# Optimization experiments

Hardware: AMD Instinct MI355X
Metric: run time of the kernel (lower is better)

Reference implementation:

```python
import jax, jax.numpy as jnp
import numpy as np

N_NODES = 100000
N_EDGES = 600000
D = 128
NUM_RELS = 200


def setup_inputs() -> dict:
    key = jax.random.key(0)
    ks = jax.random.split(key, 12)
    s = 1.0 / np.sqrt(D)
    return {
        "h": jax.random.normal(ks[0], (N_NODES, D), jnp.float32),
        "prev_h": jax.random.normal(ks[1], (N_NODES, D), jnp.float32),
        "emb_rel": jax.random.normal(ks[2], (NUM_RELS, D), jnp.float32),
        "norm": jax.random.uniform(ks[3], (N_NODES, 1), jnp.float32),
        "weight_neighbor": jax.random.normal(ks[4], (D, D), jnp.float32) * s,
        "loop_weight": jax.random.normal(ks[5], (D, D), jnp.float32) * s,
        "evolve_loop_weight": jax.random.normal(ks[6], (D, D), jnp.float32) * s,
        "skip_connect_weight": jax.random.normal(ks[7], (D, D), jnp.float32) * s,
        "skip_connect_bias": jnp.zeros((D,), jnp.float32),
        "src": jax.random.randint(ks[8], (N_EDGES,), 0, N_NODES, jnp.int64),
        "dst": jax.random.randint(ks[9], (N_EDGES,), 0, N_NODES, jnp.int64),
        "etype": jax.random.randint(ks[10], (N_EDGES,), 0, NUM_RELS, jnp.int64),
    }


def reference(h, prev_h, emb_rel, norm, weight_neighbor, loop_weight,
              evolve_loop_weight, skip_connect_weight, skip_connect_bias,
              src, dst, etype):
    n = h.shape[0]
    # self-loop message: nodes with in-degree > 0 use loop_weight, else evolve_loop_weight
    in_deg = jax.ops.segment_sum(jnp.ones_like(dst, dtype=jnp.float32), dst,
                                 num_segments=n)  # [N]
    loop_message = jnp.where(in_deg[:, None] > 0,
                             h @ loop_weight,
                             h @ evolve_loop_weight)  # [N, D]
    # skip gate from previous layer hidden state
    skip_weight = jax.nn.sigmoid(prev_h @ skip_connect_weight + skip_connect_bias)
    # msg_func: gather src node feats + relation embedding, per-edge GEMM
    msg = (h[src] + emb_rel[etype]) @ weight_neighbor  # [E, D]
    # fn.sum scatter aggregation, then apply_func: multiply by node norm
    agg = jax.ops.segment_sum(msg, dst, num_segments=n)  # [N, D]
    node_repr = agg * norm
    # skip_connect (prev_h non-empty) + self_loop branch
    node_repr = node_repr + loop_message
    node_repr = skip_weight * node_repr + (1.0 - skip_weight) * prev_h
    # activation
    return jax.nn.relu(node_repr)
```

## Files before the change

### kernel.cpp

```cpp
#include <hip/hip_runtime.h>

#define DD 128

typedef __attribute__((ext_vector_type(8))) short short8;
typedef __attribute__((ext_vector_type(4))) float f32x4;
typedef __attribute__((ext_vector_type(4))) int i32x4;

__device__ __forceinline__ unsigned short f2bf(float f) {
    union { float f; unsigned int i; } c; c.f = f;
    unsigned int x = c.i;
    return (unsigned short)((x + 0x7fffu + ((x >> 16) & 1u)) >> 16);
}
__device__ __forceinline__ float bfu(unsigned short u) {
    union { unsigned int i; float f; } c; c.i = ((unsigned int)u) << 16; return c.f;
}
__device__ __forceinline__ void gload_lds16(const void* g, void* l) {
    __builtin_amdgcn_global_load_lds(
        (const __attribute__((address_space(1))) unsigned int*)g,
        (__attribute__((address_space(3))) unsigned int*)l, 16, 0, 0);
}
__device__ __forceinline__ int idx_at(const int* p, int e, int is64) {
    return is64 ? p[2 * e] : p[e];
}
__device__ __forceinline__ int block_is64(const int* dst, int nE, int* s_flag) {
    if (threadIdx.x == 0) *s_flag = 0;
    __syncthreads();
    int w = 2 * (int)threadIdx.x + 1;
    if (threadIdx.x < 128 && w < nE && dst[w] != 0) atomicOr(s_flag, 1);
    __syncthreads();
    return !*s_flag;
}

__global__ __launch_bounds__(256) void prep_k(
    const float* __restrict__ h,
    const float* __restrict__ W0, const float* __restrict__ W1,
    const float* __restrict__ W2, const float* __restrict__ emb,
    const int* __restrict__ dst,
    unsigned short* __restrict__ hB,
    unsigned short* __restrict__ embB, unsigned short* __restrict__ Wt,
    int* __restrict__ deg, int nN, int nEmbEl, int nE) {
    int tid = threadIdx.x;
    int bid = blockIdx.x;
    int nHistB = (nE + 1023) / 1024;
    if (bid < nHistB) {
        __shared__ int s_flag;
        int is64 = block_is64(dst, nE, &s_flag);
        int e0 = bid * 1024 + tid * 4;
        #pragma unroll
        for (int j = 0; j < 4; ++j) {
            int e = e0 + j;
            if (e < nE) atomicAdd(deg + idx_at(dst, e, is64), 1);
        }
        return;
    }
    bid -= nHistB;
    int totalH = nN * DD;
    int nConvH = (totalH + 8191) / 8192;
    if (bid < nConvH) {
        int base0 = bid * 8192;
        if (base0 + 8192 <= totalH) {
            int base = base0 + tid * 8;
            f32x4 x[4][2];
            #pragma unroll
            for (int i = 0; i < 4; ++i) {
                x[i][0] = *(const f32x4*)(h + base + i * 2048);
                x[i][1] = *(const f32x4*)(h + base + i * 2048 + 4);
            }
            #pragma unroll
            for (int i = 0; i < 4; ++i) {
                short8 p;
                #pragma unroll
                for (int j = 0; j < 4; ++j) {
                    p[j]     = (short)f2bf(x[i][0][j]);
                    p[4 + j] = (short)f2bf(x[i][1][j]);
                }
                *(short8*)(hB + base + i * 2048) = p;
            }
        } else {
            #pragma unroll
            for (int i = 0; i < 4; ++i) {
                int b2 = base0 + i * 2048 + tid * 8;
                if (b2 + 8 <= totalH) {
                    f32x4 x0 = *(const f32x4*)(h + b2);
                    f32x4 x1 = *(const f32x4*)(h + b2 + 4);
                    short8 p;
                    #pragma unroll
                    for (int j = 0; j < 4; ++j) {
                        p[j]     = (short)f2bf(x0[j]);
                        p[4 + j] = (short)f2bf(x1[j]);
                    }
                    *(short8*)(hB + b2) = p;
                } else {
                    for (int j = b2; j < totalH && j < b2 + 8; ++j)
                        hB[j] = f2bf(h[j]);
                }
            }
        }
        return;
    }
    bid -= nConvH;
    if (bid < 48) {
        const float* Ws[3] = {W0, W1, W2};
        int w = bid >> 4, chunk = bid & 15;
        unsigned short* T = Wt + w * (DD * DD);
        #pragma unroll
        for (int i = 0; i < 4; ++i) {
            int t = chunk * 1024 + i * 256 + tid;
            int n = t >> 7, k = t & 127;
            T[t] = f2bf(Ws[w][k * DD + n]);
        }
        return;
    }
    bid -= 48;
    int base = bid * 2048 + tid * 8;
    if (base + 8 <= nEmbEl) {
        f32x4 x0 = *(const f32x4*)(emb + base);
        f32x4 x1 = *(const f32x4*)(emb + base + 4);
        short8 p;
        #pragma unroll
        for (int j = 0; j < 4; ++j) {
            p[j]     = (short)f2bf(x0[j]);
            p[4 + j] = (short)f2bf(x1[j]);
        }
        *(short8*)(embB + base) = p;
    } else {
        for (int j = base; j < nEmbEl; ++j) embB[j] = f2bf(emb[j]);
    }
}

__global__ __launch_bounds__(1024) void scan1_k(const int* deg, int* off, int* bsum,
                                                int nN) {
    __shared__ int s[1024];
    int t = threadIdx.x, i = blockIdx.x * 1024 + t;
    int v = (i < nN) ? deg[i] : 0;
    s[t] = v;
    __syncthreads();
    for (int d = 1; d < 1024; d <<= 1) {
        int x = (t >= d) ? s[t - d] : 0;
        __syncthreads();
        s[t] += x;
        __syncthreads();
    }
    if (i < nN) off[i] = s[t] - v;
    if (t == 1023) bsum[blockIdx.x] = s[1023];
}

__global__ __launch_bounds__(1024) void scan23_k(const int* bsum, int* off,
                                                 int* cursor, int nN, int nB) {
    __shared__ int s[1024];
    int t = threadIdx.x;
    s[t] = (t < nB) ? bsum[t] : 0;
    __syncthreads();
    for (int d = 1; d < 1024; d <<= 1) {
        int x = (t >= d) ? s[t - d] : 0;
        __syncthreads();
        s[t] += x;
        __syncthreads();
    }
    int base = (blockIdx.x == 0) ? 0 : s[blockIdx.x - 1];
    int i = blockIdx.x * 1024 + t;
    if (i < nN) {
        int o = off[i] + base;
        off[i] = o;
        cursor[i] = o;
    }
}

__global__ __launch_bounds__(256) void sort_k(const int* src, const int* dst,
                                              const int* et, int nE,
                                              int* cursor, unsigned int* edges) {
    __shared__ int s_flag;
    int is64 = block_is64(dst, nE, &s_flag);
    int e = blockIdx.x * 256 + threadIdx.x;
    if (e >= nE) return;
    int d = idx_at(dst, e, is64);
    int pos = atomicAdd(cursor + d, 1);
    edges[pos] = (unsigned int)idx_at(src, e, is64) |
                 ((unsigned int)idx_at(et, e, is64) << 17);
}

__global__ __launch_bounds__(256) void gather_k(
    const unsigned short* __restrict__ hB, const unsigned short* __restrict__ embB,
    const unsigned int* __restrict__ edges, const int* __restrict__ off,
    const int* __restrict__ deg, const float* __restrict__ normv,
    char* __restrict__ aggP, int nN) {
    int lane = threadIdx.x & 63;
    int v = blockIdx.x * 4 + (threadIdx.x >> 6);
    if (v >= nN) return;
    int slot = lane >> 4, l16 = lane & 15;
    int b = off[v], n = deg[v];
    float a[8] = {0.f, 0.f, 0.f, 0.f, 0.f, 0.f, 0.f, 0.f};
    for (int base = 0; base < n; base += 8) {
        int m0 = base + slot, m1 = base + 4 + slot;
        bool v0 = m0 < n, v1 = m1 < n;
        unsigned int w0 = 0, w1 = 0;
        if (v0) w0 = edges[b + m0];
        if (v1) w1 = edges[b + m1];
        short8 hv0, rv0, hv1, rv1;
        if (v0) {
            hv0 = *(const short8*)(hB + (size_t)(w0 & 0x1FFFFu) * DD + l16 * 8);
            rv0 = *(const short8*)(embB + (size_t)(w0 >> 17) * DD + l16 * 8);
        }
        if (v1) {
            hv1 = *(const short8*)(hB + (size_t)(w1 & 0x1FFFFu) * DD + l16 * 8);
            rv1 = *(const short8*)(embB + (size_t)(w1 >> 17) * DD + l16 * 8);
        }
        if (v0) {
            #pragma unroll
            for (int j = 0; j < 8; ++j)
                a[j] += bfu((unsigned short)hv0[j]) + bfu((unsigned short)rv0[j]);
        }
        if (v1) {
            #pragma unroll
            for (int j = 0; j < 8; ++j)
                a[j] += bfu((unsigned short)hv1[j]) + bfu((unsigned short)rv1[j]);
        }
    }
    #pragma unroll
    for (int j = 0; j < 8; ++j) {
        a[j] += __shfl_xor(a[j], 16);
        a[j] += __shfl_xor(a[j], 32);
    }
    if (slot == 0) {
        float nm = normv[v];
        short8 p;
        #pragma unroll
        for (int j = 0; j < 8; ++j) p[j] = (short)f2bf(a[j] * nm);
        *(short8*)(aggP + (size_t)v * 512 + l16 * 16) = p;
    }
}

__global__ __launch_bounds__(256, 1) void fused_k(
    const unsigned short* __restrict__ hB,
    const float* __restrict__ prevh,
    const float* __restrict__ bias,
    const char* __restrict__ aggP,
    const unsigned short* __restrict__ Wt,
    float* __restrict__ out, int nN, int nTiles) {
    extern __shared__ unsigned short lds[];
    const int lane = threadIdx.x & 63;
    const int wv = threadIdx.x >> 6;
    const int q = lane >> 4, cl = lane & 15;
    const int ncb = wv * 32;
    const int stride = gridDim.x;

    int t = blockIdx.x;
    if (t >= nTiles) return;

    short8 bn[4][2], bl[4][2], bs[4][2];
    #pragma unroll
    for (int ks = 0; ks < 4; ++ks)
        #pragma unroll
        for (int nt = 0; nt < 2; ++nt) {
            int n = (ncb + nt * 16 + cl) * DD + ks * 32 + q * 8;
            bn[ks][nt] = *(const short8*)(Wt + n);
            bl[ks][nt] = *(const short8*)(Wt + DD * DD + n);
            bs[ks][nt] = *(const short8*)(Wt + 2 * DD * DD + n);
        }
    const float b0 = bias[ncb + cl], b1 = bias[ncb + 16 + cl];

    const int r0 = lane >> 4;
    const int c16 = lane & 15;

    {
        int node_base = t * 64;
        #pragma unroll
        for (int it = 0; it < 4; ++it) {
            int r = it * 16 + wv * 4 + r0;
            int row = node_base + r; if (row > nN - 1) row = nN - 1;
            int sw = (c16 ^ (r & 15)) << 4;
            char* bptr = (char*)lds + (it * 16 + wv * 4) * 256;
            gload_lds16(aggP + (size_t)row * 512 + sw, bptr);
            gload_lds16((const char*)hB + (size_t)row * 256 + sw, bptr + 16384);
        }
        f32x4 p0[4], p1[4];
        #pragma unroll
        for (int it = 0; it < 4; ++it) {
            int pos = it * 512 + lane * 8;
            int node = node_base + wv * 16 + (pos >> 7);
            if (node > nN - 1) node = nN - 1;
            const float* g = prevh + (size_t)node * DD + (pos & 127);
            p0[it] = *(const f32x4*)g;
            p1[it] = *(const f32x4*)(g + 4);
        }
        #pragma unroll
        for (int it = 0; it < 4; ++it) {
            int pos = it * 512 + lane * 8;
            int r = wv * 16 + (pos >> 7);
            int c = (pos & 127) >> 3;
            short8 p;
            #pragma unroll
            for (int j = 0; j < 4; ++j) {
                p[j]     = (short)f2bf(p0[it][j]);
                p[4 + j] = (short)f2bf(p1[it][j]);
            }
            *(short8*)((char*)lds + 32768 + r * 256 + ((c ^ (r & 15)) << 4)) = p;
        }
    }
    __syncthreads();

    int cur = 0;
    for (;;) {
        int node_base = t * 64;
        int tn = t + stride;
        bool more = (tn < nTiles);

        f32x4 p0[4], p1[4];
        if (more) {
            int nb2 = tn * 64;
            char* dbuf = (char*)lds + (cur ^ 1) * 49152;
            #pragma unroll
            for (int it = 0; it < 4; ++it) {
                int r = it * 16 + wv * 4 + r0;
                int row = nb2 + r; if (row > nN - 1) row = nN - 1;
                int sw = (c16 ^ (r & 15)) << 4;
                char* bptr = dbuf + (it * 16 + wv * 4) * 256;
                gload_lds16(aggP + (size_t)row * 512 + sw, bptr);
                gload_lds16((const char*)hB + (size_t)row * 256 + sw, bptr + 16384);
            }
            #pragma unroll
            for (int it = 0; it < 4; ++it) {
                int pos = it * 512 + lane * 8;
                int node = nb2 + wv * 16 + (pos >> 7);
                if (node > nN - 1) node = nN - 1;
                const float* g = prevh + (size_t)node * DD + (pos & 127);
                p0[it] = *(const f32x4*)g;
                p1[it] = *(const f32x4*)(g + 4);
            }
        }

        const unsigned short* lA = lds + cur * 24576;
        const unsigned short* lH = lA + 8192;
        const unsigned short* lP = lA + 16384;

        f32x4 accM[4][2], accG[4][2];
        #pragma unroll
        for (int mt = 0; mt < 4; ++mt)
            #pragma unroll
            for (int nt = 0; nt < 2; ++nt) {
                accM[mt][nt] = (f32x4){0.f, 0.f, 0.f, 0.f};
                accG[mt][nt] = (f32x4){0.f, 0.f, 0.f, 0.f};
            }
        #pragma unroll
        for (int ks = 0; ks < 4; ++ks) {
            int swz = ((ks * 4 + q) ^ cl) << 3;
            #pragma unroll
            for (int mt = 0; mt < 4; ++mt) {
                int off = (mt * 16 + cl) * 128 + swz;
                short8 aA = *(const short8*)(lA + off);
                short8 aH = *(const short8*)(lH + off);
                short8 aP = *(const short8*)(lP + off);
                #pragma unroll
                for (int nt = 0; nt < 2; ++nt) {
                    accM[mt][nt] = __builtin_amdgcn_mfma_f32_16x16x32_bf16(
                        aA, bn[ks][nt], accM[mt][nt], 0, 0, 0);
                    accM[mt][nt] = __builtin_amdgcn_mfma_f32_16x16x32_bf16(
                        aH, bl[ks][nt], accM[mt][nt], 0, 0, 0);
                    accG[mt][nt] = __builtin_amdgcn_mfma_f32_16x16x32_bf16(
                        aP, bs[ks][nt], accG[mt][nt], 0, 0, 0);
                }
            }
        }

        #pragma unroll
        for (int mt = 0; mt < 4; ++mt) {
            #pragma unroll
            for (int r = 0; r < 4; ++r) {
                int nrow = mt * 16 + q * 4 + r;
                int node = node_base + nrow;
                if (node >= nN) continue;
                #pragma unroll
                for (int nt = 0; nt < 2; ++nt) {
                    int col = ncb + nt * 16 + cl;
                    float pv = bfu(lP[nrow * 128 +
                                      ((((col >> 3) ^ (nrow & 15)) << 3) | (col & 7))]);
                    float sg = 1.0f / (1.0f + __expf(-(accG[mt][nt][r] +
                                                       (nt ? b1 : b0))));
                    float o  = sg * accM[mt][nt][r] + (1.0f - sg) * pv;
                    out[(size_t)node * DD + col] = (o > 0.f ? o : 0.f);
                }
            }
        }

        if (more) {
            char* dbuf = (char*)lds + (cur ^ 1) * 49152;
            #pragma unroll
            for (int it = 0; it < 4; ++it) {
                int pos = it * 512 + lane * 8;
                int r = wv * 16 + (pos >> 7);
                int c = (pos & 127) >> 3;
                short8 p;
                #pragma unroll
                for (int j = 0; j < 4; ++j) {
                    p[j]     = (short)f2bf(p0[it][j]);
                    p[4 + j] = (short)f2bf(p1[it][j]);
                }
                *(short8*)(dbuf + 32768 + r * 256 + ((c ^ (r & 15)) << 4)) = p;
            }
        }
        __syncthreads();
        if (!more) break;
        cur ^= 1;
        t = tn;
    }
}

__global__ __launch_bounds__(256) void fix_k(
    const float* __restrict__ h, const float* __restrict__ prevh,
    const float* __restrict__ bias, const float* __restrict__ We,
    const float* __restrict__ Wsk, const int* __restrict__ deg,
    float* __restrict__ out, int nN, int chunk) {
    __shared__ int list[256];
    __shared__ int cnt;
    __shared__ float hrow[DD], prow[DD], res[2][DD];
    int tid = threadIdx.x;
    int base = blockIdx.x * chunk;
    for (int c = base; c < base + chunk && c < nN; c += 256) {
        if (tid == 0) cnt = 0;
        __syncthreads();
        int v = c + tid;
        if (v < nN && v < base + chunk && deg[v] == 0)
            list[atomicAdd(&cnt, 1)] = v;
        __syncthreads();
        int m = cnt;
        for (int i = 0; i < m; ++i) {
            int node = list[i];
            if (tid < DD) hrow[tid] = h[(size_t)node * DD + tid];
            else prow[tid - DD] = prevh[(size_t)node * DD + tid - DD];
            __syncthreads();
            int col = tid & (DD - 1);
            int half = tid >> 7;
            const float* W = half ? Wsk : We;
            const float* x = half ? prow : hrow;
            float s = 0.f;
            for (int k = 0; k < DD; ++k) s += x[k] * W[k * DD + col];
            res[half][col] = s;
            __syncthreads();
            if (tid < DD) {
                float sg = 1.0f / (1.0f + __expf(-(res[1][col] + bias[col])));
                float o  = sg * res[0][col] + (1.0f - sg) * prow[col];
                out[(size_t)node * DD + col] = (o > 0.f ? o : 0.f);
            }
            __syncthreads();
        }
        __syncthreads();
    }
}

extern "C" void kernel_launch(void* const* d_in, const int* in_sizes, int n_in,
                              void* d_out, int out_size, void* d_ws, size_t ws_size,
                              hipStream_t stream) {
    const float* h     = (const float*)d_in[0];
    const float* prevh = (const float*)d_in[1];
    const float* emb   = (const float*)d_in[2];
    const float* normv = (const float*)d_in[3];
    const float* Wn    = (const float*)d_in[4];
    const float* Wl    = (const float*)d_in[5];
    const float* We    = (const float*)d_in[6];
    const float* Wsk   = (const float*)d_in[7];
    const float* bias  = (const float*)d_in[8];
    const int* src   = (const int*)d_in[9];
    const int* dst   = (const int*)d_in[10];
    const int* etype = (const int*)d_in[11];

    int nN = in_sizes[3];
    int nE = in_sizes[9];
    int nEmbEl = in_sizes[2];

    char* w = (char*)d_ws;
    size_t o = 0;
    unsigned short* Wt = (unsigned short*)(w + o);  o += 3 * DD * DD * 2;
    unsigned short* embB = (unsigned short*)(w + o); o += ((size_t)nEmbEl * 2 + 255) & ~(size_t)255;
    int* deg    = (int*)(w + o);  o += ((size_t)nN * 4 + 15) & ~(size_t)15;
    int* offA   = (int*)(w + o);  o += ((size_t)nN * 4 + 15) & ~(size_t)15;
    int* cursor = (int*)(w + o);  o += ((size_t)nN * 4 + 15) & ~(size_t)15;
    int* bsum   = (int*)(w + o);  o += 4096;
    unsigned int* edges = (unsigned int*)(w + o); o += ((size_t)nE * 4 + 15) & ~(size_t)15;
    unsigned short* hB = (unsigned short*)(w + o);

    int totalH = nN * DD;
    int nConvH = (totalH + 8191) / 8192;
    int nEmbB  = (nEmbEl + 2047) / 2048;
    int nHistB = (nE + 1023) / 1024;
    int nB = (nN + 1023) / 1024;
    int nTiles = (nN + 63) / 64;
    int fgrid2 = nTiles < 256 ? nTiles : 256;

    hipMemsetAsync(deg, 0, (size_t)nN * sizeof(int), stream);
    prep_k<<<nHistB + nConvH + 48 + nEmbB, 256, 0, stream>>>(
        h, Wn, Wl, Wsk, emb, dst, hB, embB, Wt, deg, nN, nEmbEl, nE);
    scan1_k<<<nB, 1024, 0, stream>>>(deg, offA, bsum, nN);
    scan23_k<<<nB, 1024, 0, stream>>>(bsum, offA, cursor, nN, nB);
    sort_k<<<(nE + 255) / 256, 256, 0, stream>>>(src, dst, etype, nE, cursor, edges);
    gather_k<<<(nN + 3) / 4, 256, 0, stream>>>(hB, embB, edges, offA, deg, normv,
                                               (char*)d_out, nN);
    fused_k<<<fgrid2, 256, 98304, stream>>>(hB, prevh, bias, (const char*)d_out,
                                            Wt, (float*)d_out, nN, nTiles);
    int fgrid = 256;
    int chunk = ((nN + fgrid * 256 - 1) / (fgrid * 256)) * 256;
    fix_k<<<fgrid, 256, 0, stream>>>(h, prevh, bias, We, Wsk, deg, (float*)d_out,
                                     nN, chunk);
    (void)ws_size; (void)n_in; (void)out_size;
}
```

Baseline: 311.8 us.

## Replace global-atomic edge sort with two-pass bucketed counting sort; shrink fused tiles

The per-edge scatter with a global atomic per destination node is replaced by a two-pass sort. The first pass does a block-local histogram over 128-node buckets, makes one global atomic per bucket and writes to a staging array. The second pass scatters within each bucket using LDS atomics. This cuts global atomic contention and makes the edge writes more local, at the cost of an extra pass over the edges and an extra staging buffer. Separately, the fused GEMM kernel moves to 32-row tiles with half the LDS and a 512-block grid, so two blocks can be resident per CU.

```diff
diff --git a/kernel.cpp b/kernel.cpp
--- a/kernel.cpp
+++ b/kernel.cpp
@@ -1,6 +1,7 @@
 #include <hip/hip_runtime.h>
 
 #define DD 128
+#define SCHUNK 4096
 
 typedef __attribute__((ext_vector_type(8))) short short8;
 typedef __attribute__((ext_vector_type(4))) float f32x4;
@@ -146,7 +147,7 @@
 }
 
 __global__ __launch_bounds__(1024) void scan23_k(const int* bsum, int* off,
-                                                 int* cursor, int nN, int nB) {
+                                                 int* cursorB, int nN, int nB) {
     __shared__ int s[1024];
     int t = threadIdx.x;
     s[t] = (t < nB) ? bsum[t] : 0;
@@ -162,21 +163,67 @@
     if (i < nN) {
         int o = off[i] + base;
         off[i] = o;
-        cursor[i] = o;
-    }
-}
-
-__global__ __launch_bounds__(256) void sort_k(const int* src, const int* dst,
-                                              const int* et, int nE,
-                                              int* cursor, unsigned int* edges) {
+        if ((i & 127) == 0) cursorB[i >> 7] = o;
+    }
+}
+
+__global__ __launch_bounds__(256) void sort1_k(
+    const int* __restrict__ src, const int* __restrict__ dst,
+    const int* __restrict__ et, int nE, int nBuck,
+    int* __restrict__ cursorB, unsigned int* __restrict__ staging) {
+    __shared__ int hist[2048];
+    __shared__ int rbase[2048];
+    __shared__ unsigned short ranks[SCHUNK];
     __shared__ int s_flag;
+    int tid = threadIdx.x;
     int is64 = block_is64(dst, nE, &s_flag);
-    int e = blockIdx.x * 256 + threadIdx.x;
-    if (e >= nE) return;
-    int d = idx_at(dst, e, is64);
-    int pos = atomicAdd(cursor + d, 1);
-    edges[pos] = (unsigned int)idx_at(src, e, is64) |
-                 ((unsigned int)idx_at(et, e, is64) << 17);
+    for (int i = tid; i < nBuck; i += 256) hist[i] = 0;
+    __syncthreads();
+    int cbase = blockIdx.x * SCHUNK;
+    #pragma unroll
+    for (int j = 0; j < SCHUNK / 256; ++j) {
+        int e = cbase + j * 256 + tid;
+        if (e < nE) {
+            int d = idx_at(dst, e, is64);
+            ranks[j * 256 + tid] = (unsigned short)atomicAdd(&hist[d >> 7], 1);
+        }
+    }
+    __syncthreads();
+    for (int b = tid; b < nBuck; b += 256) {
+        int c = hist[b];
+        if (c) rbase[b] = atomicAdd(cursorB + b, c);
+    }
+    __syncthreads();
+    #pragma unroll
+    for (int j = 0; j < SCHUNK / 256; ++j) {
+        int e = cbase + j * 256 + tid;
+        if (e < nE) {
+            int d = idx_at(dst, e, is64);
+            unsigned int wd = (unsigned int)idx_at(src, e, is64) |
+                              ((unsigned int)idx_at(et, e, is64) << 17) |
+                              ((unsigned int)(d & 127) << 25);
+            staging[rbase[d >> 7] + (int)ranks[j * 256 + tid]] = wd;
+        }
+    }
+}
+
+__global__ __launch_bounds__(256) void sort2_k(
+    const unsigned int* __restrict__ staging, const int* __restrict__ off,
+    int nN, int nE, unsigned int* __restrict__ edges) {
+    __shared__ int cur[128];
+    int b = blockIdx.x;
+    int first = b << 7;
+    int tid = threadIdx.x;
+    if (tid < 128 && first + tid < nN) cur[tid] = off[first + tid];
+    int rStart = off[first];
+    int nxt = first + 128;
+    int rEnd = (nxt < nN) ? off[nxt] : nE;
+    __syncthreads();
+    for (int i = rStart + tid; i < rEnd; i += 256) {
+        unsigned int wd = staging[i];
+        int p = atomicAdd(&cur[wd >> 25], 1);
+        edges[p] = wd & 0x1FFFFFFu;
+    }
 }
 
 __global__ __launch_bounds__(256) void gather_k(
@@ -230,7 +277,7 @@
     }
 }
 
-__global__ __launch_bounds__(256, 1) void fused_k(
+__global__ __launch_bounds__(256, 2) void fused_k(
     const unsigned short* __restrict__ hB,
     const float* __restrict__ prevh,
     const float* __restrict__ bias,
@@ -263,30 +310,30 @@
     const int c16 = lane & 15;
 
     {
-        int node_base = t * 64;
-        #pragma unroll
-        for (int it = 0; it < 4; ++it) {
+        int node_base = t * 32;
+        #pragma unroll
+        for (int it = 0; it < 2; ++it) {
             int r = it * 16 + wv * 4 + r0;
             int row = node_base + r; if (row > nN - 1) row = nN - 1;
             int sw = (c16 ^ (r & 15)) << 4;
             char* bptr = (char*)lds + (it * 16 + wv * 4) * 256;
             gload_lds16(aggP + (size_t)row * 512 + sw, bptr);
-            gload_lds16((const char*)hB + (size_t)row * 256 + sw, bptr + 16384);
-        }
-        f32x4 p0[4], p1[4];
-        #pragma unroll
-        for (int it = 0; it < 4; ++it) {
+            gload_lds16((const char*)hB + (size_t)row * 256 + sw, bptr + 8192);
+        }
+        f32x4 p0[2], p1[2];
+        #pragma unroll
+        for (int it = 0; it < 2; ++it) {
             int pos = it * 512 + lane * 8;
-            int node = node_base + wv * 16 + (pos >> 7);
+            int node = node_base + wv * 8 + (pos >> 7);
             if (node > nN - 1) node = nN - 1;
             const float* g = prevh + (size_t)node * DD + (pos & 127);
             p0[it] = *(const f32x4*)g;
             p1[it] = *(const f32x4*)(g + 4);
         }
         #pragma unroll
-        for (int it = 0; it < 4; ++it) {
+        for (int it = 0; it < 2; ++it) {
             int pos = it * 512 + lane * 8;
-            int r = wv * 16 + (pos >> 7);
+            int r = wv * 8 + (pos >> 7);
             int c = (pos & 127) >> 3;
             short8 p;
             #pragma unroll
@@ -294,34 +341,34 @@
                 p[j]     = (short)f2bf(p0[it][j]);
                 p[4 + j] = (short)f2bf(p1[it][j]);
             }
-            *(short8*)((char*)lds + 32768 + r * 256 + ((c ^ (r & 15)) << 4)) = p;
+            *(short8*)((char*)lds + 16384 + r * 256 + ((c ^ (r & 15)) << 4)) = p;
         }
     }
     __syncthreads();
 
     int cur = 0;
     for (;;) {
-        int node_base = t * 64;
+        int node_base = t * 32;
         int tn = t + stride;
         bool more = (tn < nTiles);
 
-        f32x4 p0[4], p1[4];
+        f32x4 p0[2], p1[2];
         if (more) {
-            int nb2 = tn * 64;
-            char* dbuf = (char*)lds + (cur ^ 1) * 49152;
-            #pragma unroll
-            for (int it = 0; it < 4; ++it) {
+            int nb2 = tn * 32;
+            char* dbuf = (char*)lds + (cur ^ 1) * 24576;
+            #pragma unroll
+            for (int it = 0; it < 2; ++it) {
                 int r = it * 16 + wv * 4 + r0;
                 int row = nb2 + r; if (row > nN - 1) row = nN - 1;
                 int sw = (c16 ^ (r & 15)) << 4;
                 char* bptr = dbuf + (it * 16 + wv * 4) * 256;
                 gload_lds16(aggP + (size_t)row * 512 + sw, bptr);
-                gload_lds16((const char*)hB + (size_t)row * 256 + sw, bptr + 16384);
-            }
-            #pragma unroll
-            for (int it = 0; it < 4; ++it) {
+                gload_lds16((const char*)hB + (size_t)row * 256 + sw, bptr + 8192);
+            }
+            #pragma unroll
+            for (int it = 0; it < 2; ++it) {
                 int pos = it * 512 + lane * 8;
-                int node = nb2 + wv * 16 + (pos >> 7);
+                int node = nb2 + wv * 8 + (pos >> 7);
                 if (node > nN - 1) node = nN - 1;
                 const float* g = prevh + (size_t)node * DD + (pos & 127);
                 p0[it] = *(const f32x4*)g;
@@ -329,13 +376,13 @@
             }
         }
 
-        const unsigned short* lA = lds + cur * 24576;
-        const unsigned short* lH = lA + 8192;
-        const unsigned short* lP = lA + 16384;
-
-        f32x4 accM[4][2], accG[4][2];
-        #pragma unroll
-        for (int mt = 0; mt < 4; ++mt)
+        const unsigned short* lA = lds + cur * 12288;
+        const unsigned short* lH = lA + 4096;
+        const unsigned short* lP = lA + 8192;
+
+        f32x4 accM[2][2], accG[2][2];
+        #pragma unroll
+        for (int mt = 0; mt < 2; ++mt)
             #pragma unroll
             for (int nt = 0; nt < 2; ++nt) {
                 accM[mt][nt] = (f32x4){0.f, 0.f, 0.f, 0.f};
@@ -345,7 +392,7 @@
         for (int ks = 0; ks < 4; ++ks) {
             int swz = ((ks * 4 + q) ^ cl) << 3;
             #pragma unroll
-            for (int mt = 0; mt < 4; ++mt) {
+            for (int mt = 0; mt < 2; ++mt) {
                 int off = (mt * 16 + cl) * 128 + swz;
                 short8 aA = *(const short8*)(lA + off);
                 short8 aH = *(const short8*)(lH + off);
@@ -363,7 +410,7 @@
         }
 
         #pragma unroll
-        for (int mt = 0; mt < 4; ++mt) {
+        for (int mt = 0; mt < 2; ++mt) {
             #pragma unroll
             for (int r = 0; r < 4; ++r) {
                 int nrow = mt * 16 + q * 4 + r;
@@ -383,11 +430,11 @@
         }
 
         if (more) {
-            char* dbuf = (char*)lds + (cur ^ 1) * 49152;
-            #pragma unroll
-            for (int it = 0; it < 4; ++it) {
+            char* dbuf = (char*)lds + (cur ^ 1) * 24576;
+            #pragma unroll
+            for (int it = 0; it < 2; ++it) {
                 int pos = it * 512 + lane * 8;
-                int r = wv * 16 + (pos >> 7);
+                int r = wv * 8 + (pos >> 7);
                 int c = (pos & 127) >> 3;
                 short8 p;
                 #pragma unroll
@@ -395,7 +442,7 @@
                     p[j]     = (short)f2bf(p0[it][j]);
                     p[4 + j] = (short)f2bf(p1[it][j]);
                 }
-                *(short8*)(dbuf + 32768 + r * 256 + ((c ^ (r & 15)) << 4)) = p;
+                *(short8*)(dbuf + 16384 + r * 256 + ((c ^ (r & 15)) << 4)) = p;
             }
         }
         __syncthreads();
@@ -471,11 +518,12 @@
     size_t o = 0;
     unsigned short* Wt = (unsigned short*)(w + o);  o += 3 * DD * DD * 2;
     unsigned short* embB = (unsigned short*)(w + o); o += ((size_t)nEmbEl * 2 + 255) & ~(size_t)255;
-    int* deg    = (int*)(w + o);  o += ((size_t)nN * 4 + 15) & ~(size_t)15;
-    int* offA   = (int*)(w + o);  o += ((size_t)nN * 4 + 15) & ~(size_t)15;
-    int* cursor = (int*)(w + o);  o += ((size_t)nN * 4 + 15) & ~(size_t)15;
-    int* bsum   = (int*)(w + o);  o += 4096;
-    unsigned int* edges = (unsigned int*)(w + o); o += ((size_t)nE * 4 + 15) & ~(size_t)15;
+    int* deg     = (int*)(w + o);  o += ((size_t)nN * 4 + 15) & ~(size_t)15;
+    int* offA    = (int*)(w + o);  o += ((size_t)nN * 4 + 15) & ~(size_t)15;
+    int* cursorB = (int*)(w + o);  o += 8192;
+    int* bsum    = (int*)(w + o);  o += 4096;
+    unsigned int* edges   = (unsigned int*)(w + o); o += ((size_t)nE * 4 + 15) & ~(size_t)15;
+    unsigned int* staging = (unsigned int*)(w + o); o += ((size_t)nE * 4 + 15) & ~(size_t)15;
     unsigned short* hB = (unsigned short*)(w + o);
 
     int totalH = nN * DD;
@@ -483,18 +531,21 @@
     int nEmbB  = (nEmbEl + 2047) / 2048;
     int nHistB = (nE + 1023) / 1024;
     int nB = (nN + 1023) / 1024;
-    int nTiles = (nN + 63) / 64;
-    int fgrid2 = nTiles < 256 ? nTiles : 256;
+    int nBuck = (nN + 127) / 128;
+    int nTiles = (nN + 31) / 32;
+    int fgrid2 = nTiles < 512 ? nTiles : 512;
 
     hipMemsetAsync(deg, 0, (size_t)nN * sizeof(int), stream);
     prep_k<<<nHistB + nConvH + 48 + nEmbB, 256, 0, stream>>>(
         h, Wn, Wl, Wsk, emb, dst, hB, embB, Wt, deg, nN, nEmbEl, nE);
     scan1_k<<<nB, 1024, 0, stream>>>(deg, offA, bsum, nN);
-    scan23_k<<<nB, 1024, 0, stream>>>(bsum, offA, cursor, nN, nB);
-    sort_k<<<(nE + 255) / 256, 256, 0, stream>>>(src, dst, etype, nE, cursor, edges);
+    scan23_k<<<nB, 1024, 0, stream>>>(bsum, offA, cursorB, nN, nB);
+    sort1_k<<<(nE + SCHUNK - 1) / SCHUNK, 256, 0, stream>>>(
+        src, dst, etype, nE, nBuck, cursorB, staging);
+    sort2_k<<<nBuck, 256, 0, stream>>>(staging, offA, nN, nE, edges);
     gather_k<<<(nN + 3) / 4, 256, 0, stream>>>(hB, embB, edges, offA, deg, normv,
                                                (char*)d_out, nN);
-    fused_k<<<fgrid2, 256, 98304, stream>>>(hB, prevh, bias, (const char*)d_out,
+    fused_k<<<fgrid2, 256, 49152, stream>>>(hB, prevh, bias, (const char*)d_out,
                                             Wt, (float*)d_out, nN, nTiles);
     int fgrid = 256;
     int chunk = ((nN + fgrid * 256 - 1) / (fgrid * 256)) * 256;
```

Measured after the change: 292.0 us. 1.07x faster.
